# Performance work log

Hardware: AMD Instinct MI355X
Metric: run time of the kernel (lower is better)

## Reference

```python
import jax, jax.numpy as jnp
import numpy as np

B = 131072   # batch of states (e.g. ODE integrator batch)
S = 2        # state_dim (q, p)
H = 512      # hidden_dim
E = 8        # action_embedding_dim


def setup_inputs() -> dict:
    key = jax.random.key(0)
    ks = jax.random.split(key, 8)
    sc = lambda n: 1.0 / np.sqrt(n)
    return {
        "t": 0,  # unused time scalar (odeint signature)
        "state": jax.random.normal(ks[0], (B, S), dtype=jnp.float32),
        "action_emb": jax.random.normal(ks[1], (B, E), dtype=jnp.float32),
        # H_net: Linear(S,H) -> Softplus -> Linear(H,H) -> Softplus -> Linear(H,1)
        "W1": jax.random.normal(ks[2], (S, H), dtype=jnp.float32) * sc(S),
        "b1": jnp.zeros((H,), dtype=jnp.float32),
        "W2": jax.random.normal(ks[3], (H, H), dtype=jnp.float32) * sc(H),
        "b2": jnp.zeros((H,), dtype=jnp.float32),
        "W3": jax.random.normal(ks[4], (H, 1), dtype=jnp.float32) * sc(H),
        "b3": jnp.zeros((1,), dtype=jnp.float32),
        "log_damping": jnp.asarray(-1.0, dtype=jnp.float32),
        # G_net: Linear(E, S//2)
        "Gw": jax.random.normal(ks[5], (E, S // 2), dtype=jnp.float32) * sc(E),
        "Gb": jnp.zeros((S // 2,), dtype=jnp.float32),
    }


def reference(t, state, action_emb, W1, b1, W2, b2, W3, b3, log_damping, Gw, Gb):
    # Hamiltonian net: scalar H per state; sum over batch so jax.grad gives
    # per-sample dH/dstate in one pass (equivalent to autograd.grad with ones cotangent).
    def H_sum(s):
        h = jax.nn.softplus(s @ W1 + b1)       # [B, H]
        h = jax.nn.softplus(h @ W2 + b2)       # [B, H]
        return jnp.sum(h @ W3 + b3)            # scalar

    dH_dstate = jax.grad(H_sum)(state)         # [B, S]
    dH_dq = dH_dstate[..., 0:1]                # [B, 1]
    dH_dp = dH_dstate[..., 1:2]                # [B, 1]

    damping = jnp.exp(log_damping)
    G_u = action_emb @ Gw + Gb                 # [B, 1]

    dq_dt = dH_dp
    dp_dt = -dH_dq - damping * dH_dp + G_u
    return jnp.concatenate([dq_dt, dp_dt], axis=-1)  # [B, S]
```

## Files before the change

kernel.cpp:

```cpp
#include <hip/hip_runtime.h>

typedef __bf16 bf16x8 __attribute__((ext_vector_type(8)));
typedef float f32x4 __attribute__((ext_vector_type(4)));
typedef float f32x16 __attribute__((ext_vector_type(16)));
typedef unsigned short u16x8 __attribute__((ext_vector_type(8)));

#define DEVI static __device__ __forceinline__

DEVI unsigned short f2b(float x) {
  __bf16 b = (__bf16)x;
  return __builtin_bit_cast(unsigned short, b);
}

__global__ __launch_bounds__(256) void pack_w2_kernel(
    const float* __restrict__ W2, unsigned short* __restrict__ p1,
    unsigned short* __restrict__ p2) {
  int idx = blockIdx.x * 256 + threadIdx.x;
  int which = idx >> 18;
  int i = idx & 262143;
  int j = i & 7;
  int l = (i >> 3) & 63;
  if (which == 0) {
    int t0 = (i >> 9) & 15;
    int s = i >> 13;
    p1[i] = f2b(W2[(s * 16 + (l >> 5) * 8 + j) * 512 + t0 * 32 + (l & 31)]);
  } else {
    int t0 = (i >> 9) & 31;
    int s = i >> 14;
    p2[i] = f2b(W2[(t0 * 16 + (l & 15)) * 512 + s * 32 + (l >> 4) * 8 + j]);
  }
}

__global__ __launch_bounds__(256, 2) void phm_kernel(
    const float* __restrict__ state, const float* __restrict__ action_emb,
    const float* __restrict__ W1, const float* __restrict__ b1,
    const float* __restrict__ b2, const float* __restrict__ W3,
    const float* __restrict__ log_damping, const float* __restrict__ Gw,
    const float* __restrict__ Gb, const unsigned short* __restrict__ packB1,
    const unsigned short* __restrict__ packB2, float* __restrict__ out) {
  __shared__ unsigned short buf[64 * 512];
  __shared__ float W1s[1024];
  __shared__ float b1s[512];
  __shared__ float b2s[512];
  __shared__ float W3s[512];
  __shared__ float st[128];
  __shared__ float part[4][64][2];

  const int t = threadIdx.x;
  const int lane = t & 63;
  const int wid = t >> 6;
  const int l15 = lane & 15;
  const int l4 = lane >> 4;
  const int l31 = lane & 31;
  const int l5 = lane >> 5;
  const long row0 = (long)blockIdx.x * 64;
  char* bufc = reinterpret_cast<char*>(buf);

  for (int i = t; i < 512; i += 256) {
    W1s[i] = W1[i];
    W1s[512 + i] = W1[512 + i];
    b1s[i] = b1[i];
    b2s[i] = b2[i];
    W3s[i] = W3[i];
  }
  if (t < 128) st[t] = state[row0 * 2 + t];
  __syncthreads();

  for (int it = 0; it < 16; ++it) {
    int page = it * 4 + wid;
    int s = page >> 1, rt = page & 1;
    int row = rt * 32 + l31;
    int k0 = s * 16 + l5 * 8;
    float s0 = st[row * 2], s1 = st[row * 2 + 1];
    u16x8 pk;
#pragma unroll
    for (int j = 0; j < 8; ++j) {
      int c = k0 + j;
      float z = fmaf(s0, W1s[c], fmaf(s1, W1s[512 + c], b1s[c]));
      float e = __expf(-fabsf(z));
      float h = fmaxf(z, 0.f) + __logf(1.f + e);
      pk[j] = f2b(h);
    }
    *reinterpret_cast<u16x8*>(bufc + page * 1024 + lane * 16) = pk;
  }
  __syncthreads();

  f32x16 acc1[2][4];
#pragma unroll
  for (int rt = 0; rt < 2; ++rt)
#pragma unroll
    for (int ct = 0; ct < 4; ++ct)
#pragma unroll
      for (int r = 0; r < 16; ++r) acc1[rt][ct][r] = 0.f;

#pragma unroll 4
  for (int s = 0; s < 32; ++s) {
    bf16x8 af[2];
#pragma unroll
    for (int rt = 0; rt < 2; ++rt)
      af[rt] = __builtin_bit_cast(
          bf16x8, *reinterpret_cast<const int4*>(
                      bufc + (s * 2 + rt) * 1024 + lane * 16));
    bf16x8 bfr[4];
#pragma unroll
    for (int ct = 0; ct < 4; ++ct)
      bfr[ct] = __builtin_bit_cast(
          bf16x8, *reinterpret_cast<const int4*>(
                      packB1 + ((s * 16 + wid * 4 + ct) * 64 + lane) * 8));
#pragma unroll
    for (int rt = 0; rt < 2; ++rt)
#pragma unroll
      for (int ct = 0; ct < 4; ++ct)
        acc1[rt][ct] = __builtin_amdgcn_mfma_f32_32x32x16_bf16(
            af[rt], bfr[ct], acc1[rt][ct], 0, 0, 0);
  }
  __syncthreads();

#pragma unroll
  for (int rt = 0; rt < 2; ++rt) {
#pragma unroll
    for (int ct = 0; ct < 4; ++ct) {
      int c = wid * 128 + ct * 32 + l31;
      float w3 = W3s[c], bb = b2s[c];
      int pbase = (c >> 5) * 4096 + (c & 7) * 2;
      int oct = (l31 >> 3);
#pragma unroll
      for (int reg = 0; reg < 16; ++reg) {
        int row = rt * 32 + (reg & 3) + 8 * (reg >> 2) + 4 * l5;
        float z2 = acc1[rt][ct][reg] + bb;
        float sg = __builtin_amdgcn_rcpf(1.f + __expf(-z2));
        unsigned short u = f2b(w3 * sg);
        int lane2 = (row & 15) + 16 * oct;
        int slot = lane2 ^ (lane2 >> 4);
        *reinterpret_cast<unsigned short*>(
            bufc + pbase + (row >> 4) * 1024 + slot * 16) = u;
      }
    }
  }
  __syncthreads();

  float2 sv[16];
#pragma unroll
  for (int rt2 = 0; rt2 < 4; ++rt2)
#pragma unroll
    for (int jj = 0; jj < 4; ++jj) {
      int r = rt2 * 16 + l4 * 4 + jj;
      sv[rt2 * 4 + jj] = *reinterpret_cast<const float2*>(&st[r * 2]);
    }

  f32x4 acc2[4][8];
#pragma unroll
  for (int a = 0; a < 4; ++a)
#pragma unroll
    for (int b = 0; b < 8; ++b)
#pragma unroll
      for (int r = 0; r < 4; ++r) acc2[a][b][r] = 0.f;

  const int rslot = (lane ^ (lane >> 4)) * 16;
#pragma unroll 2
  for (int s2 = 0; s2 < 16; ++s2) {
    bf16x8 af[4];
#pragma unroll
    for (int rt2 = 0; rt2 < 4; ++rt2)
      af[rt2] = __builtin_bit_cast(
          bf16x8, *reinterpret_cast<const int4*>(
                      bufc + s2 * 4096 + rt2 * 1024 + rslot));
    bf16x8 bfr[8];
#pragma unroll
    for (int ct2 = 0; ct2 < 8; ++ct2)
      bfr[ct2] = __builtin_bit_cast(
          bf16x8, *reinterpret_cast<const int4*>(
                      packB2 + ((s2 * 32 + wid * 8 + ct2) * 64 + lane) * 8));
#pragma unroll
    for (int rt2 = 0; rt2 < 4; ++rt2)
#pragma unroll
      for (int ct2 = 0; ct2 < 8; ++ct2)
        acc2[rt2][ct2] = __builtin_amdgcn_mfma_f32_16x16x32_bf16(
            af[rt2], bfr[ct2], acc2[rt2][ct2], 0, 0, 0);
  }

  float p0[16], p1v[16];
#pragma unroll
  for (int i = 0; i < 16; ++i) { p0[i] = 0.f; p1v[i] = 0.f; }

#pragma unroll
  for (int ct2 = 0; ct2 < 8; ++ct2) {
    int hc = wid * 128 + ct2 * 16 + l15;
    float w10 = W1s[hc], w11 = W1s[512 + hc], bb = b1s[hc];
#pragma unroll
    for (int rt2 = 0; rt2 < 4; ++rt2) {
#pragma unroll
      for (int jj = 0; jj < 4; ++jj) {
        float2 sp = sv[rt2 * 4 + jj];
        float z1 = fmaf(sp.x, w10, fmaf(sp.y, w11, bb));
        float sg = __builtin_amdgcn_rcpf(1.f + __expf(-z1));
        float dz1 = acc2[rt2][ct2][jj] * sg;
        p0[rt2 * 4 + jj] = fmaf(dz1, w10, p0[rt2 * 4 + jj]);
        p1v[rt2 * 4 + jj] = fmaf(dz1, w11, p1v[rt2 * 4 + jj]);
      }
    }
  }

#pragma unroll
  for (int i = 0; i < 16; ++i) {
    float a = p0[i], b = p1v[i];
    for (int m = 1; m < 16; m <<= 1) {
      a += __shfl_xor(a, m, 64);
      b += __shfl_xor(b, m, 64);
    }
    p0[i] = a;
    p1v[i] = b;
  }
  if (l15 == 0) {
#pragma unroll
    for (int rt2 = 0; rt2 < 4; ++rt2)
#pragma unroll
      for (int jj = 0; jj < 4; ++jj) {
        int r = rt2 * 16 + l4 * 4 + jj;
        part[wid][r][0] = p0[rt2 * 4 + jj];
        part[wid][r][1] = p1v[rt2 * 4 + jj];
      }
  }
  __syncthreads();

  if (t < 64) {
    long grow = row0 + t;
    float g0 = part[0][t][0] + part[1][t][0] + part[2][t][0] + part[3][t][0];
    float g1 = part[0][t][1] + part[1][t][1] + part[2][t][1] + part[3][t][1];
    const float4 ae0 = reinterpret_cast<const float4*>(action_emb)[grow * 2];
    const float4 ae1 = reinterpret_cast<const float4*>(action_emb)[grow * 2 + 1];
    float gu = Gb[0];
    gu = fmaf(ae0.x, Gw[0], gu);
    gu = fmaf(ae0.y, Gw[1], gu);
    gu = fmaf(ae0.z, Gw[2], gu);
    gu = fmaf(ae0.w, Gw[3], gu);
    gu = fmaf(ae1.x, Gw[4], gu);
    gu = fmaf(ae1.y, Gw[5], gu);
    gu = fmaf(ae1.z, Gw[6], gu);
    gu = fmaf(ae1.w, Gw[7], gu);
    float damping = __expf(log_damping[0]);
    float2 o;
    o.x = g1;
    o.y = -g0 - damping * g1 + gu;
    reinterpret_cast<float2*>(out)[grow] = o;
  }
}

extern "C" void kernel_launch(void* const* d_in, const int* in_sizes, int n_in,
                              void* d_out, int out_size, void* d_ws,
                              size_t ws_size, hipStream_t stream) {
  const float* state = (const float*)d_in[1];
  const float* action_emb = (const float*)d_in[2];
  const float* W1 = (const float*)d_in[3];
  const float* b1 = (const float*)d_in[4];
  const float* W2 = (const float*)d_in[5];
  const float* b2 = (const float*)d_in[6];
  const float* W3 = (const float*)d_in[7];
  const float* log_damping = (const float*)d_in[9];
  const float* Gw = (const float*)d_in[10];
  const float* Gb = (const float*)d_in[11];
  float* out = (float*)d_out;

  unsigned short* p1 = (unsigned short*)d_ws;
  unsigned short* p2 = p1 + 262144;

  pack_w2_kernel<<<dim3(2048), dim3(256), 0, stream>>>(W2, p1, p2);
  phm_kernel<<<dim3(2048), dim3(256), 0, stream>>>(
      state, action_emb, W1, b1, b2, W3, log_damping, Gw, Gb, p1, p2, out);
}
```

Baseline: 177.6 us.

## Split work over 8 waves, fold log2e into weights, use transpose-style shuffle reduction

The fused Hamiltonian-gradient kernel moves to 512 threads per block (8 waves), and each wave handles half as many output column tiles in both MFMA GEMMs. The second GEMM is split into two chunks so fewer accumulators are live at once. W1, b1 and b2 are pre-scaled by log2(e) so the softplus and sigmoid can use native exp2/log2, with a single ln2 rescale at the end. The per-row cross-lane reduction becomes a butterfly transpose that leaves one finished value per lane. The aim is more latency hiding and fewer transcendental and shuffle instructions, but the 512,4 launch bound sharply caps registers and may cause spills, while LDS usage still limits blocks per CU.

```diff
diff --git a/kernel.cpp b/kernel.cpp
--- a/kernel.cpp
+++ b/kernel.cpp
@@ -10,6 +10,21 @@
 DEVI unsigned short f2b(float x) {
   __bf16 b = (__bf16)x;
   return __builtin_bit_cast(unsigned short, b);
+}
+
+DEVI float ex2(float x) {
+#if __has_builtin(__builtin_amdgcn_exp2f)
+  return __builtin_amdgcn_exp2f(x);
+#else
+  return __expf(x * 0.69314718f);
+#endif
+}
+DEVI float lg2(float x) {
+#if __has_builtin(__builtin_amdgcn_logf)
+  return __builtin_amdgcn_logf(x);
+#else
+  return __logf(x) * 1.44269504f;
+#endif
 }
 
 __global__ __launch_bounds__(256) void pack_w2_kernel(
@@ -31,7 +46,7 @@
   }
 }
 
-__global__ __launch_bounds__(256, 2) void phm_kernel(
+__global__ __launch_bounds__(512, 4) void phm_kernel(
     const float* __restrict__ state, const float* __restrict__ action_emb,
     const float* __restrict__ W1, const float* __restrict__ b1,
     const float* __restrict__ b2, const float* __restrict__ W3,
@@ -44,7 +59,7 @@
   __shared__ float b2s[512];
   __shared__ float W3s[512];
   __shared__ float st[128];
-  __shared__ float part[4][64][2];
+  __shared__ float2 part2[8][64];
 
   const int t = threadIdx.x;
   const int lane = t & 63;
@@ -55,19 +70,21 @@
   const int l5 = lane >> 5;
   const long row0 = (long)blockIdx.x * 64;
   char* bufc = reinterpret_cast<char*>(buf);
-
-  for (int i = t; i < 512; i += 256) {
-    W1s[i] = W1[i];
-    W1s[512 + i] = W1[512 + i];
-    b1s[i] = b1[i];
-    b2s[i] = b2[i];
+  const float LOG2E = 1.44269504f;
+
+  for (int i = t; i < 512; i += 512) {
+    W1s[i] = W1[i] * LOG2E;
+    W1s[512 + i] = W1[512 + i] * LOG2E;
+    b1s[i] = b1[i] * LOG2E;
+    b2s[i] = b2[i] * LOG2E;
     W3s[i] = W3[i];
   }
   if (t < 128) st[t] = state[row0 * 2 + t];
   __syncthreads();
 
-  for (int it = 0; it < 16; ++it) {
-    int page = it * 4 + wid;
+#pragma unroll
+  for (int it = 0; it < 8; ++it) {
+    int page = it * 8 + wid;
     int s = page >> 1, rt = page & 1;
     int row = rt * 32 + l31;
     int k0 = s * 16 + l5 * 8;
@@ -76,24 +93,23 @@
 #pragma unroll
     for (int j = 0; j < 8; ++j) {
       int c = k0 + j;
-      float z = fmaf(s0, W1s[c], fmaf(s1, W1s[512 + c], b1s[c]));
-      float e = __expf(-fabsf(z));
-      float h = fmaxf(z, 0.f) + __logf(1.f + e);
-      pk[j] = f2b(h);
+      float zp = fmaf(s0, W1s[c], fmaf(s1, W1s[512 + c], b1s[c]));
+      float hp = fmaxf(zp, 0.f) + lg2(1.f + ex2(-fabsf(zp)));
+      pk[j] = f2b(hp);
     }
     *reinterpret_cast<u16x8*>(bufc + page * 1024 + lane * 16) = pk;
   }
   __syncthreads();
 
-  f32x16 acc1[2][4];
+  f32x16 acc1[2][2];
 #pragma unroll
   for (int rt = 0; rt < 2; ++rt)
 #pragma unroll
-    for (int ct = 0; ct < 4; ++ct)
+    for (int ct = 0; ct < 2; ++ct)
 #pragma unroll
       for (int r = 0; r < 16; ++r) acc1[rt][ct][r] = 0.f;
 
-#pragma unroll 4
+#pragma unroll 2
   for (int s = 0; s < 32; ++s) {
     bf16x8 af[2];
 #pragma unroll
@@ -101,34 +117,34 @@
       af[rt] = __builtin_bit_cast(
           bf16x8, *reinterpret_cast<const int4*>(
                       bufc + (s * 2 + rt) * 1024 + lane * 16));
-    bf16x8 bfr[4];
-#pragma unroll
-    for (int ct = 0; ct < 4; ++ct)
+    bf16x8 bfr[2];
+#pragma unroll
+    for (int ct = 0; ct < 2; ++ct)
       bfr[ct] = __builtin_bit_cast(
           bf16x8, *reinterpret_cast<const int4*>(
-                      packB1 + ((s * 16 + wid * 4 + ct) * 64 + lane) * 8));
+                      packB1 + ((s * 16 + wid * 2 + ct) * 64 + lane) * 8));
 #pragma unroll
     for (int rt = 0; rt < 2; ++rt)
 #pragma unroll
-      for (int ct = 0; ct < 4; ++ct)
+      for (int ct = 0; ct < 2; ++ct)
         acc1[rt][ct] = __builtin_amdgcn_mfma_f32_32x32x16_bf16(
             af[rt], bfr[ct], acc1[rt][ct], 0, 0, 0);
   }
   __syncthreads();
 
 #pragma unroll
-  for (int rt = 0; rt < 2; ++rt) {
-#pragma unroll
-    for (int ct = 0; ct < 4; ++ct) {
-      int c = wid * 128 + ct * 32 + l31;
-      float w3 = W3s[c], bb = b2s[c];
-      int pbase = (c >> 5) * 4096 + (c & 7) * 2;
-      int oct = (l31 >> 3);
+  for (int ct = 0; ct < 2; ++ct) {
+    int c = (wid * 2 + ct) * 32 + l31;
+    float w3 = W3s[c], bbL = b2s[c];
+    int pbase = (c >> 5) * 4096 + (c & 7) * 2;
+    int oct = (c >> 3) & 3;
+#pragma unroll
+    for (int rt = 0; rt < 2; ++rt) {
 #pragma unroll
       for (int reg = 0; reg < 16; ++reg) {
         int row = rt * 32 + (reg & 3) + 8 * (reg >> 2) + 4 * l5;
-        float z2 = acc1[rt][ct][reg] + bb;
-        float sg = __builtin_amdgcn_rcpf(1.f + __expf(-z2));
+        float e = ex2(-(acc1[rt][ct][reg] + bbL));
+        float sg = __builtin_amdgcn_rcpf(1.f + e);
         unsigned short u = f2b(w3 * sg);
         int lane2 = (row & 15) + 16 * oct;
         int slot = lane2 ^ (lane2 >> 4);
@@ -139,94 +155,133 @@
   }
   __syncthreads();
 
-  float2 sv[16];
-#pragma unroll
-  for (int rt2 = 0; rt2 < 4; ++rt2)
-#pragma unroll
-    for (int jj = 0; jj < 4; ++jj) {
-      int r = rt2 * 16 + l4 * 4 + jj;
-      sv[rt2 * 4 + jj] = *reinterpret_cast<const float2*>(&st[r * 2]);
-    }
-
-  f32x4 acc2[4][8];
-#pragma unroll
-  for (int a = 0; a < 4; ++a)
-#pragma unroll
-    for (int b = 0; b < 8; ++b)
-#pragma unroll
-      for (int r = 0; r < 4; ++r) acc2[a][b][r] = 0.f;
+  float p0[16], p1v[16];
+#pragma unroll
+  for (int i = 0; i < 16; ++i) { p0[i] = 0.f; p1v[i] = 0.f; }
 
   const int rslot = (lane ^ (lane >> 4)) * 16;
+#pragma unroll
+  for (int chunk = 0; chunk < 2; ++chunk) {
+    f32x4 acc2[4][2];
+#pragma unroll
+    for (int a = 0; a < 4; ++a)
+#pragma unroll
+      for (int b = 0; b < 2; ++b)
+#pragma unroll
+        for (int r = 0; r < 4; ++r) acc2[a][b][r] = 0.f;
+
 #pragma unroll 2
-  for (int s2 = 0; s2 < 16; ++s2) {
-    bf16x8 af[4];
-#pragma unroll
-    for (int rt2 = 0; rt2 < 4; ++rt2)
-      af[rt2] = __builtin_bit_cast(
-          bf16x8, *reinterpret_cast<const int4*>(
-                      bufc + s2 * 4096 + rt2 * 1024 + rslot));
-    bf16x8 bfr[8];
-#pragma unroll
-    for (int ct2 = 0; ct2 < 8; ++ct2)
-      bfr[ct2] = __builtin_bit_cast(
-          bf16x8, *reinterpret_cast<const int4*>(
-                      packB2 + ((s2 * 32 + wid * 8 + ct2) * 64 + lane) * 8));
-#pragma unroll
-    for (int rt2 = 0; rt2 < 4; ++rt2)
-#pragma unroll
-      for (int ct2 = 0; ct2 < 8; ++ct2)
-        acc2[rt2][ct2] = __builtin_amdgcn_mfma_f32_16x16x32_bf16(
-            af[rt2], bfr[ct2], acc2[rt2][ct2], 0, 0, 0);
-  }
-
-  float p0[16], p1v[16];
-#pragma unroll
-  for (int i = 0; i < 16; ++i) { p0[i] = 0.f; p1v[i] = 0.f; }
-
-#pragma unroll
-  for (int ct2 = 0; ct2 < 8; ++ct2) {
-    int hc = wid * 128 + ct2 * 16 + l15;
-    float w10 = W1s[hc], w11 = W1s[512 + hc], bb = b1s[hc];
+    for (int s2 = 0; s2 < 16; ++s2) {
+      bf16x8 af[4];
+#pragma unroll
+      for (int rt2 = 0; rt2 < 4; ++rt2)
+        af[rt2] = __builtin_bit_cast(
+            bf16x8, *reinterpret_cast<const int4*>(
+                        bufc + s2 * 4096 + rt2 * 1024 + rslot));
+      bf16x8 bfr[2];
+#pragma unroll
+      for (int cc = 0; cc < 2; ++cc)
+        bfr[cc] = __builtin_bit_cast(
+            bf16x8,
+            *reinterpret_cast<const int4*>(
+                packB2 + ((s2 * 32 + wid * 4 + chunk * 2 + cc) * 64 + lane) * 8));
+#pragma unroll
+      for (int rt2 = 0; rt2 < 4; ++rt2)
+#pragma unroll
+        for (int cc = 0; cc < 2; ++cc)
+          acc2[rt2][cc] = __builtin_amdgcn_mfma_f32_16x16x32_bf16(
+              af[rt2], bfr[cc], acc2[rt2][cc], 0, 0, 0);
+    }
 #pragma unroll
     for (int rt2 = 0; rt2 < 4; ++rt2) {
-#pragma unroll
-      for (int jj = 0; jj < 4; ++jj) {
-        float2 sp = sv[rt2 * 4 + jj];
-        float z1 = fmaf(sp.x, w10, fmaf(sp.y, w11, bb));
-        float sg = __builtin_amdgcn_rcpf(1.f + __expf(-z1));
-        float dz1 = acc2[rt2][ct2][jj] * sg;
-        p0[rt2 * 4 + jj] = fmaf(dz1, w10, p0[rt2 * 4 + jj]);
-        p1v[rt2 * 4 + jj] = fmaf(dz1, w11, p1v[rt2 * 4 + jj]);
+      float2 rv[4];
+#pragma unroll
+      for (int jj = 0; jj < 4; ++jj)
+        rv[jj] = *reinterpret_cast<const float2*>(
+            &st[(rt2 * 16 + l4 * 4 + jj) * 2]);
+#pragma unroll
+      for (int cc = 0; cc < 2; ++cc) {
+        int hc = wid * 64 + (chunk * 2 + cc) * 16 + l15;
+        float w10L = W1s[hc], w11L = W1s[512 + hc], bbL = b1s[hc];
+#pragma unroll
+        for (int jj = 0; jj < 4; ++jj) {
+          float z1L = fmaf(rv[jj].x, w10L, fmaf(rv[jj].y, w11L, bbL));
+          float sg = __builtin_amdgcn_rcpf(1.f + ex2(-z1L));
+          float dz1 = acc2[rt2][cc][jj] * sg;
+          p0[rt2 * 4 + jj] = fmaf(dz1, w10L, p0[rt2 * 4 + jj]);
+          p1v[rt2 * 4 + jj] = fmaf(dz1, w11L, p1v[rt2 * 4 + jj]);
+        }
       }
     }
   }
 
-#pragma unroll
-  for (int i = 0; i < 16; ++i) {
-    float a = p0[i], b = p1v[i];
-    for (int m = 1; m < 16; m <<= 1) {
-      a += __shfl_xor(a, m, 64);
-      b += __shfl_xor(b, m, 64);
-    }
-    p0[i] = a;
-    p1v[i] = b;
-  }
-  if (l15 == 0) {
-#pragma unroll
-    for (int rt2 = 0; rt2 < 4; ++rt2)
-#pragma unroll
-      for (int jj = 0; jj < 4; ++jj) {
-        int r = rt2 * 16 + l4 * 4 + jj;
-        part[wid][r][0] = p0[rt2 * 4 + jj];
-        part[wid][r][1] = p1v[rt2 * 4 + jj];
-      }
+  float a8[8], b8[8];
+  {
+    bool bb = (l15 & 1) != 0;
+#pragma unroll
+    for (int m = 0; m < 8; ++m) {
+      float ka = bb ? p0[2 * m + 1] : p0[2 * m];
+      float sa = bb ? p0[2 * m] : p0[2 * m + 1];
+      a8[m] = ka + __shfl_xor(sa, 1, 64);
+      float kb = bb ? p1v[2 * m + 1] : p1v[2 * m];
+      float sb = bb ? p1v[2 * m] : p1v[2 * m + 1];
+      b8[m] = kb + __shfl_xor(sb, 1, 64);
+    }
+  }
+  float a4[4], b4[4];
+  {
+    bool bb = (l15 & 2) != 0;
+#pragma unroll
+    for (int m = 0; m < 4; ++m) {
+      float ka = bb ? a8[2 * m + 1] : a8[2 * m];
+      float sa = bb ? a8[2 * m] : a8[2 * m + 1];
+      a4[m] = ka + __shfl_xor(sa, 2, 64);
+      float kb = bb ? b8[2 * m + 1] : b8[2 * m];
+      float sb = bb ? b8[2 * m] : b8[2 * m + 1];
+      b4[m] = kb + __shfl_xor(sb, 2, 64);
+    }
+  }
+  float a2[2], b2v[2];
+  {
+    bool bb = (l15 & 4) != 0;
+#pragma unroll
+    for (int m = 0; m < 2; ++m) {
+      float ka = bb ? a4[2 * m + 1] : a4[2 * m];
+      float sa = bb ? a4[2 * m] : a4[2 * m + 1];
+      a2[m] = ka + __shfl_xor(sa, 4, 64);
+      float kb = bb ? b4[2 * m + 1] : b4[2 * m];
+      float sb = bb ? b4[2 * m] : b4[2 * m + 1];
+      b2v[m] = kb + __shfl_xor(sb, 4, 64);
+    }
+  }
+  float a1, b1r;
+  {
+    bool bb = (l15 & 8) != 0;
+    float ka = bb ? a2[1] : a2[0];
+    float sa = bb ? a2[0] : a2[1];
+    a1 = ka + __shfl_xor(sa, 8, 64);
+    float kb = bb ? b2v[1] : b2v[0];
+    float sb = bb ? b2v[0] : b2v[1];
+    b1r = kb + __shfl_xor(sb, 8, 64);
+  }
+  {
+    int r = (l15 >> 2) * 16 + l4 * 4 + (l15 & 3);
+    part2[wid][r] = make_float2(a1, b1r);
   }
   __syncthreads();
 
   if (t < 64) {
     long grow = row0 + t;
-    float g0 = part[0][t][0] + part[1][t][0] + part[2][t][0] + part[3][t][0];
-    float g1 = part[0][t][1] + part[1][t][1] + part[2][t][1] + part[3][t][1];
+    float g0 = 0.f, g1 = 0.f;
+#pragma unroll
+    for (int w = 0; w < 8; ++w) {
+      float2 pp = part2[w][t];
+      g0 += pp.x;
+      g1 += pp.y;
+    }
+    const float LN2 = 0.69314718f;
+    g0 *= LN2;
+    g1 *= LN2;
     const float4 ae0 = reinterpret_cast<const float4*>(action_emb)[grow * 2];
     const float4 ae1 = reinterpret_cast<const float4*>(action_emb)[grow * 2 + 1];
     float gu = Gb[0];
@@ -265,6 +320,6 @@
   unsigned short* p2 = p1 + 262144;
 
   pack_w2_kernel<<<dim3(2048), dim3(256), 0, stream>>>(W2, p1, p2);
-  phm_kernel<<<dim3(2048), dim3(256), 0, stream>>>(
+  phm_kernel<<<dim3(2048), dim3(512), 0, stream>>>(
       state, action_emb, W1, b1, b2, W3, log_damping, Gw, Gb, p1, p2, out);
 }
```

Result: faster. 155.2 us (-12.6%).
